# Kernel optimization log

Measured on AMD Instinct MI355X. Metric: run time of the kernel, lower is better.

Reference implementation:

```python
import jax, jax.numpy as jnp
import numpy as np

B, S, D = 4, 2048, 1024
EPS = 1e-6


def setup_inputs() -> dict:
    key = jax.random.key(0)
    ks = jax.random.split(key, 9)
    s = 1.0 / np.sqrt(D)
    return {
        "context": jax.random.normal(ks[0], (B, S, D), jnp.float32),
        "eos_mask": jax.random.randint(ks[1], (B, S, S), 0, 2, dtype=jnp.int32),
        "prior": jax.random.uniform(ks[2], (B, S, S), jnp.float32),
        "Wq": jax.random.uniform(ks[3], (D, D), jnp.float32, -s, s),
        "bq": jax.random.uniform(ks[4], (D,), jnp.float32, -s, s),
        "Wk": jax.random.uniform(ks[5], (D, D), jnp.float32, -s, s),
        "bk": jax.random.uniform(ks[6], (D,), jnp.float32, -s, s),
        "gamma": jnp.ones((D,), jnp.float32),
        "beta": jnp.zeros((D,), jnp.float32),
    }


def reference(context, eos_mask, prior, Wq, bq, Wk, bk, gamma, beta):
    d = context.shape[-1]
    seq = context.shape[1]

    # LayerNorm with torch's unbiased std (Bessel correction)
    mean = jnp.mean(context, axis=-1, keepdims=True)
    var = jnp.sum((context - mean) ** 2, axis=-1, keepdims=True) / (d - 1)
    x = gamma * (context - mean) / (jnp.sqrt(var) + EPS) + beta

    q = x @ Wq + bq  # linear_query
    k = x @ Wk + bk  # linear_key

    scores = jnp.einsum("bid,bjd->bij", q, k) / d  # note: /d, not /sqrt(d)

    idx = jnp.arange(seq)
    band = jnp.abs(idx[:, None] - idx[None, :]) == 1      # a + c (tridiagonal off-diagonals)
    sup = (idx[None, :] - idx[:, None]) == 1              # a (superdiagonal)
    strict_upper = idx[:, None] < idx[None, :]            # triu(ones) - eye
    eye = idx[:, None] == idx[None, :]

    mask = (eos_mask != 0) & band[None]                   # eos_mask & (a + c)
    scores = jnp.where(mask, scores, -1e9)
    na = jax.nn.softmax(scores, axis=-1)
    na = jnp.sqrt(na * jnp.swapaxes(na, -1, -2) + 1e-9)
    na = prior + (1.0 - prior) * na                       # hier_add_index branch

    # t = log(na+eps).masked_fill(a==0,0) @ triu  ==  cumsum along last axis
    t = jnp.where(sup[None], jnp.log(na + 1e-9), 0.0)
    t = jnp.cumsum(t, axis=-1)
    # g = triu @ t  ==  reversed cumsum along axis -2
    g = jnp.cumsum(t[..., ::-1, :], axis=-2)[..., ::-1, :]
    g = jnp.where(strict_upper[None], jnp.exp(g), 0.0)

    g_attn = g + jnp.swapaxes(g, -1, -2) + jnp.where(eye[None], na, 1e-9)
    return (g_attn, na)
```

## Files before the change

kernel.cpp:

```cpp
#include <hip/hip_runtime.h>
#include <hip/hip_bf16.h>
#include <cmath>

#define BB 4
#define SS 2048
#define DD 1024
#define BS (BB*SS)
constexpr float EPS = 1e-6f;

typedef __attribute__((ext_vector_type(8))) short short8;
typedef __attribute__((ext_vector_type(4))) float floatx4;

__device__ inline float bf2f(unsigned short u) {
    unsigned v = ((unsigned)u) << 16;
    float f; __builtin_memcpy(&f, &v, 4);
    return f;
}

__global__ __launch_bounds__(256)
void prep_kernel(const float* __restrict__ Wq, const float* __restrict__ Wk,
                 const float* __restrict__ bq, const float* __restrict__ bk,
                 __hip_bfloat16* __restrict__ Wb, float* __restrict__ u,
                 float* __restrict__ v, float* __restrict__ cs,
                 float* __restrict__ sacc) {
    int blk = blockIdx.x;
    if (blk < 2048) {
        int idx = blk * 256 + threadIdx.x;
        const int half = DD * DD / 4;
        const float* src = (idx < half) ? Wk : Wq;
        int off = (idx < half) ? idx : idx - half;
        float4 val = ((const float4*)src)[off];
        union { ushort4 uu; __hip_bfloat16 h[4]; } pk;
        pk.h[0] = __float2bfloat16(val.x);
        pk.h[1] = __float2bfloat16(val.y);
        pk.h[2] = __float2bfloat16(val.z);
        pk.h[3] = __float2bfloat16(val.w);
        ((ushort4*)Wb)[idx] = pk.uu;
    } else if (blk < 2561) {
        int gid = (blk - 2048) * 4 + (threadIdx.x >> 6);
        int lane = threadIdx.x & 63;
        if (gid > 2048) return;
        const float* row; const float* vec; float* outp;
        if (gid < 1024)      { row = Wq + (size_t)gid * DD;          vec = bk; outp = u + gid; }
        else if (gid < 2048) { row = Wk + (size_t)(gid - 1024) * DD; vec = bq; outp = v + (gid - 1024); }
        else                 { row = bq;                             vec = bk; outp = cs; }
        float s = 0.f;
        #pragma unroll
        for (int k = 0; k < 4; ++k) {
            float4 a = ((const float4*)row)[lane * 4 + k];
            float4 b = ((const float4*)vec)[lane * 4 + k];
            s += a.x * b.x + a.y * b.y + a.z * b.z + a.w * b.w;
        }
        #pragma unroll
        for (int off = 32; off; off >>= 1) s += __shfl_down(s, off);
        if (lane == 0) *outp = s;
    } else {
        int idx = (blk - 2561) * 1024 + threadIdx.x * 4;
        *(float4*)(sacc + idx) = make_float4(0.f, 0.f, 0.f, 0.f);
    }
}

__global__ __launch_bounds__(256)
void ln_kernel(const float* __restrict__ ctx, const float* __restrict__ gamma,
               const float* __restrict__ beta, const float* __restrict__ u,
               const float* __restrict__ v, const float* __restrict__ cs,
               __hip_bfloat16* __restrict__ xo, float* __restrict__ alpha,
               float* __restrict__ betav) {
    int row = blockIdx.x;
    int t = threadIdx.x;
    const float* r = ctx + (size_t)row * DD;
    float4 val = ((const float4*)r)[t];
    float s1 = val.x + val.y + val.z + val.w;
    float s2 = val.x*val.x + val.y*val.y + val.z*val.z + val.w*val.w;
    #pragma unroll
    for (int off = 32; off; off >>= 1) {
        s1 += __shfl_down(s1, off);
        s2 += __shfl_down(s2, off);
    }
    __shared__ float ls1[4], ls2[4];
    int wid = t >> 6, lane = t & 63;
    if (lane == 0) { ls1[wid] = s1; ls2[wid] = s2; }
    __syncthreads();
    if (t == 0) {
        float a = ls1[0] + ls1[1] + ls1[2] + ls1[3];
        float b = ls2[0] + ls2[1] + ls2[2] + ls2[3];
        float mean = a / DD;
        float var = (b - a * a / DD) / (DD - 1);
        ls1[0] = mean;
        ls2[0] = 1.0f / (sqrtf(var) + EPS);
    }
    __syncthreads();
    float mean = ls1[0], rstd = ls2[0];
    float4 g = ((const float4*)gamma)[t];
    float4 be = ((const float4*)beta)[t];
    float nx0 = g.x * (val.x - mean) * rstd + be.x;
    float nx1 = g.y * (val.y - mean) * rstd + be.y;
    float nx2 = g.z * (val.z - mean) * rstd + be.z;
    float nx3 = g.w * (val.w - mean) * rstd + be.w;
    union { ushort4 uu; __hip_bfloat16 h[4]; } pk;
    pk.h[0] = __float2bfloat16(nx0);
    pk.h[1] = __float2bfloat16(nx1);
    pk.h[2] = __float2bfloat16(nx2);
    pk.h[3] = __float2bfloat16(nx3);
    ((ushort4*)(xo + (size_t)row * DD))[t] = pk.uu;
    float4 u4 = ((const float4*)u)[t];
    float4 v4 = ((const float4*)v)[t];
    float du = nx0 * u4.x + nx1 * u4.y + nx2 * u4.z + nx3 * u4.w;
    float dv = nx0 * v4.x + nx1 * v4.y + nx2 * v4.z + nx3 * v4.w;
    #pragma unroll
    for (int off = 32; off; off >>= 1) {
        du += __shfl_down(du, off);
        dv += __shfl_down(dv, off);
    }
    __syncthreads();
    if (lane == 0) { ls1[wid] = du; ls2[wid] = dv; }
    __syncthreads();
    if (t == 0) {
        alpha[row] = ls1[0] + ls1[1] + ls1[2] + ls1[3] + *cs;
        betav[row] = ls2[0] + ls2[1] + ls2[2] + ls2[3];
    }
}

__global__ __launch_bounds__(256)
void gemm64_mfma(const __hip_bfloat16* __restrict__ A,
                 const __hip_bfloat16* __restrict__ B,
                 __hip_bfloat16* __restrict__ C, int ldc) {
    __shared__ short As[64 * 64];
    __shared__ short Bs[64 * 64];
    int tid = threadIdx.x;
    int wave = tid >> 6;
    int lane = tid & 63;
    int q = lane >> 4, m16 = lane & 15;
    int srow = lane >> 3;
    int skoff = (lane & 7) * 8;

    const __hip_bfloat16* gA = A + ((size_t)blockIdx.x * 64 + wave * 16 + srow) * DD + skoff;
    const __hip_bfloat16* gB = B + ((size_t)blockIdx.y * 64 + wave * 16 + srow) * DD + skoff;
    short* lA0 = As + (wave * 16) * 64;
    short* lA1 = As + (wave * 16 + 8) * 64;
    short* lB0 = Bs + (wave * 16) * 64;
    short* lB1 = Bs + (wave * 16 + 8) * 64;

    floatx4 acc[4] = {};
    for (int k0 = 0; k0 < DD; k0 += 64) {
        __builtin_amdgcn_global_load_lds(
            (const __attribute__((address_space(1))) void*)(gA + k0),
            (__attribute__((address_space(3))) void*)(lA0), 16, 0, 0);
        __builtin_amdgcn_global_load_lds(
            (const __attribute__((address_space(1))) void*)(gA + k0 + 8 * DD),
            (__attribute__((address_space(3))) void*)(lA1), 16, 0, 0);
        __builtin_amdgcn_global_load_lds(
            (const __attribute__((address_space(1))) void*)(gB + k0),
            (__attribute__((address_space(3))) void*)(lB0), 16, 0, 0);
        __builtin_amdgcn_global_load_lds(
            (const __attribute__((address_space(1))) void*)(gB + k0 + 8 * DD),
            (__attribute__((address_space(3))) void*)(lB1), 16, 0, 0);
        __syncthreads();
        #pragma unroll
        for (int h = 0; h < 2; ++h) {
            short8 af = *(const short8*)(As + (wave * 16 + m16) * 64 + h * 32 + q * 8);
            #pragma unroll
            for (int c = 0; c < 4; ++c) {
                short8 bf_ = *(const short8*)(Bs + (c * 16 + m16) * 64 + h * 32 + q * 8);
                acc[c] = __builtin_amdgcn_mfma_f32_16x16x32_bf16(af, bf_, acc[c], 0, 0, 0);
            }
        }
        __syncthreads();
    }
    #pragma unroll
    for (int c = 0; c < 4; ++c) {
        int gcol = blockIdx.y * 64 + c * 16 + m16;
        #pragma unroll
        for (int e = 0; e < 4; ++e) {
            int grow = blockIdx.x * 64 + wave * 16 + q * 4 + e;
            C[(size_t)grow * ldc + gcol] = __float2bfloat16(acc[c][e]);
        }
    }
}

#define TM 128
#define TN 128
#define TK 32
__global__ __launch_bounds__(256)
void gemm2_fused(const __hip_bfloat16* __restrict__ A,
                 const __hip_bfloat16* __restrict__ B,
                 float* __restrict__ sacc) {
    __shared__ short smem[18432];
    short* As = smem;
    short* Bs = smem + TM * TK;
    int tid = threadIdx.x;
    int wave = tid >> 6;
    int lane = tid & 63;
    int wm = wave >> 1, wn = wave & 1;
    int q = lane >> 4, m16 = lane & 15;

    int srow = lane >> 2;
    int skoff = (lane & 3) * 8;
    const __hip_bfloat16* gA = A + ((size_t)blockIdx.x * TM + wave * 32 + srow) * DD + skoff;
    const __hip_bfloat16* gB = B + ((size_t)blockIdx.y * TN + wave * 32 + srow) * DD + skoff;
    short* lAbase = As + (wave * 32) * TK;
    short* lBbase = Bs + (wave * 32) * TK;

    floatx4 acc[4][4] = {};

    for (int k0 = 0; k0 < DD; k0 += TK) {
        __builtin_amdgcn_global_load_lds(
            (const __attribute__((address_space(1))) void*)(gA + k0),
            (__attribute__((address_space(3))) void*)(lAbase), 16, 0, 0);
        __builtin_amdgcn_global_load_lds(
            (const __attribute__((address_space(1))) void*)(gA + k0 + 16 * DD),
            (__attribute__((address_space(3))) void*)(lAbase + 16 * TK), 16, 0, 0);
        __builtin_amdgcn_global_load_lds(
            (const __attribute__((address_space(1))) void*)(gB + k0),
            (__attribute__((address_space(3))) void*)(lBbase), 16, 0, 0);
        __builtin_amdgcn_global_load_lds(
            (const __attribute__((address_space(1))) void*)(gB + k0 + 16 * DD),
            (__attribute__((address_space(3))) void*)(lBbase + 16 * TK), 16, 0, 0);
        __syncthreads();
        short8 af[4], bf_[4];
        #pragma unroll
        for (int r = 0; r < 4; ++r)
            af[r] = *(const short8*)(As + (wm * 64 + r * 16 + m16) * TK + q * 8);
        #pragma unroll
        for (int c = 0; c < 4; ++c)
            bf_[c] = *(const short8*)(Bs + (wn * 64 + c * 16 + m16) * TK + q * 8);
        #pragma unroll
        for (int r = 0; r < 4; ++r)
            #pragma unroll
            for (int c = 0; c < 4; ++c)
                acc[r][c] = __builtin_amdgcn_mfma_f32_16x16x32_bf16(af[r], bf_[c], acc[r][c], 0, 0, 0);
        __syncthreads();
    }

    short* EP = smem + wave * 4608;
    #pragma unroll
    for (int r = 0; r < 4; ++r)
        #pragma unroll
        for (int c = 0; c < 4; ++c)
            #pragma unroll
            for (int e = 0; e < 4; ++e) {
                __hip_bfloat16 hv = __float2bfloat16(acc[r][c][e]);
                EP[(r * 16 + q * 4 + e) * 72 + c * 16 + m16] = *(short*)&hv;
            }

    int rl = lane;
    int growZ = blockIdx.x * TM + wm * 64 + rl;
    int gcol0 = blockIdx.y * TN + wn * 64;
    float zf[64];
    #pragma unroll
    for (int c8 = 0; c8 < 8; ++c8) {
        short8 zz = *(const short8*)(EP + rl * 72 + c8 * 8);
        #pragma unroll
        for (int e = 0; e < 8; ++e) zf[c8 * 8 + e] = bf2f((unsigned short)zz[e]);
    }
    if (growZ + 1 < BS) {
        const short8* px = (const short8*)(A + (size_t)(growZ + 1) * DD + gcol0);
        float sup = 0.f;
        #pragma unroll
        for (int c8 = 0; c8 < 8; ++c8) {
            short8 xx = px[c8];
            #pragma unroll
            for (int e = 0; e < 8; ++e) sup += zf[c8 * 8 + e] * bf2f((unsigned short)xx[e]);
        }
        atomicAdd(&sacc[growZ], sup);
    }
    if (growZ >= 1) {
        const short8* px = (const short8*)(A + (size_t)(growZ - 1) * DD + gcol0);
        float sub = 0.f;
        #pragma unroll
        for (int c8 = 0; c8 < 8; ++c8) {
            short8 xx = px[c8];
            #pragma unroll
            for (int e = 0; e < 8; ++e) sub += zf[c8 * 8 + e] * bf2f((unsigned short)xx[e]);
        }
        atomicAdd(&sacc[BS + growZ], sub);
    }
}

__global__ __launch_bounds__(256)
void softmax_kernel(const float* __restrict__ sacc, const int* __restrict__ eos,
                    const float* __restrict__ alpha, const float* __restrict__ betav,
                    float* __restrict__ vsub, float* __restrict__ vsup,
                    float* __restrict__ wuni) {
    int gw = blockIdx.x * 256 + threadIdx.x;
    int i = gw & (SS - 1);
    float a = alpha[gw];
    float ssup = 0.f, ssub = 0.f;
    if (i < SS - 1) ssup = (sacc[gw] + a + betav[gw + 1]) * (1.0f / DD);
    if (i > 0)      ssub = (sacc[BS + gw] + a + betav[gw - 1]) * (1.0f / DD);
    bool msub = (i > 0) && (eos[(size_t)gw * SS + (i - 1)] != 0);
    bool msup = (i < SS - 1) && (eos[(size_t)gw * SS + (i + 1)] != 0);
    float vs, vp, w;
    if (msub && msup) {
        float mx = fmaxf(ssub, ssup);
        float e1 = expf(ssub - mx), e2 = expf(ssup - mx);
        float inv = 1.0f / (e1 + e2);
        vs = e1 * inv; vp = e2 * inv; w = 0.f;
    } else if (msub) { vs = 1.f; vp = 0.f; w = 0.f; }
    else if (msup)   { vs = 0.f; vp = 1.f; w = 0.f; }
    else             { vs = vp = w = 1.0f / SS; }
    vsub[gw] = vs; vsup[gw] = vp; wuni[gw] = w;
}

__global__ __launch_bounds__(256)
void scan_kernel(const float* __restrict__ prior, const float* __restrict__ vsub,
                 const float* __restrict__ vsup, double* __restrict__ Lc) {
    int b = blockIdx.x;
    int t = threadIdx.x;
    double loc[8];
    double s = 0.0;
    #pragma unroll
    for (int k = 0; k < 8; ++k) {
        int tt = t * 8 + k;
        double Lv = 0.0;
        if (tt < SS - 1) {
            float pr = prior[((size_t)(b * SS + tt)) * SS + tt + 1];
            float na2 = sqrtf(vsup[b * SS + tt] * vsub[b * SS + tt + 1] + 1e-9f);
            float P = pr + (1.f - pr) * na2;
            Lv = log((double)P + 1e-9);
        }
        loc[k] = Lv; s += Lv;
    }
    __shared__ double sa[256], sb[256];
    sa[t] = s;
    __syncthreads();
    double* src = sa; double* dst = sb;
    for (int off = 1; off < 256; off <<= 1) {
        double v = src[t];
        if (t >= off) v += src[t - off];
        __syncthreads();
        dst[t] = v;
        __syncthreads();
        double* tmp = src; src = dst; dst = tmp;
    }
    double run = (t == 0) ? 0.0 : src[t - 1];
    #pragma unroll
    for (int k = 0; k < 8; ++k) {
        int idx = t * 8 + k;
        Lc[b * SS + idx] = run;
        run += loc[k];
    }
}

__global__ __launch_bounds__(256)
void out_kernel(const float* __restrict__ prior, const float* __restrict__ vsub,
                const float* __restrict__ vsup, const float* __restrict__ wuni,
                const double* __restrict__ Lc, float* __restrict__ out_g,
                float* __restrict__ out_na) {
    size_t gid = (size_t)blockIdx.x * 256 + threadIdx.x;
    int jt = (int)(gid & 511);
    int row = (int)(gid >> 9);
    int i = row & (SS - 1);
    int b = row >> 11;
    int j0 = jt * 4;
    size_t base = (size_t)row * SS + j0;
    float4 pr4 = *(const float4*)(prior + base);
    float4 wj4 = *(const float4*)(wuni + b * SS + j0);
    float pra[4] = {pr4.x, pr4.y, pr4.z, pr4.w};
    float wja[4] = {wj4.x, wj4.y, wj4.z, wj4.w};
    float wi = wuni[row];
    double Lci = Lc[row];
    const double* Lcb = Lc + b * SS;
    float nav[4], gv[4];
    #pragma unroll
    for (int c = 0; c < 4; ++c) {
        int j = j0 + c;
        float prod;
        if (j == i - 1)      prod = vsub[row] * vsup[row - 1];
        else if (j == i + 1) prod = vsup[row] * vsub[row + 1];
        else if (j == i)     prod = wi * wi;
        else                 prod = wi * wja[c];
        float na2 = sqrtf(prod + 1e-9f);
        float p = pra[c];
        float na3 = p + (1.f - p) * na2;
        nav[c] = na3;
        if (j == i) {
            gv[c] = na3;
        } else {
            double d = (j > i) ? (Lcb[j] - Lci) : (Lci - Lcb[j]);
            gv[c] = expf((float)d) + 1e-9f;
        }
    }
    *(float4*)(out_g + base) = make_float4(gv[0], gv[1], gv[2], gv[3]);
    *(float4*)(out_na + base) = make_float4(nav[0], nav[1], nav[2], nav[3]);
}

extern "C" void kernel_launch(void* const* d_in, const int* in_sizes, int n_in,
                              void* d_out, int out_size, void* d_ws, size_t ws_size,
                              hipStream_t stream) {
    const float* ctx   = (const float*)d_in[0];
    const int*   eos   = (const int*)d_in[1];
    const float* prior = (const float*)d_in[2];
    const float* Wq    = (const float*)d_in[3];
    const float* bq    = (const float*)d_in[4];
    const float* Wk    = (const float*)d_in[5];
    const float* bk    = (const float*)d_in[6];
    const float* gamma = (const float*)d_in[7];
    const float* beta  = (const float*)d_in[8];

    float* out_g  = (float*)d_out;
    float* out_na = out_g + (size_t)BB * SS * SS;

    char* ws = (char*)d_ws;
    size_t o = 0;
    __hip_bfloat16* x  = (__hip_bfloat16*)(ws + o); o += (size_t)BS * DD * 2;
    __hip_bfloat16* Wb = (__hip_bfloat16*)(ws + o); o += (size_t)2 * DD * DD * 2;
    __hip_bfloat16* Mt = (__hip_bfloat16*)(ws + o); o += (size_t)DD * DD * 2;
    double* Lc   = (double*)(ws + o); o += (size_t)BS * 8;
    float* u     = (float*)(ws + o);  o += DD * 4;
    float* v     = (float*)(ws + o);  o += DD * 4;
    float* cs    = (float*)(ws + o);  o += 64;
    float* alpha = (float*)(ws + o);  o += (size_t)BS * 4;
    float* betav = (float*)(ws + o);  o += (size_t)BS * 4;
    float* vsub  = (float*)(ws + o);  o += (size_t)BS * 4;
    float* vsup  = (float*)(ws + o);  o += (size_t)BS * 4;
    float* wuni  = (float*)(ws + o);  o += (size_t)BS * 4;
    float* sacc  = (float*)(ws + o);  o += (size_t)2 * BS * 4;

    __hip_bfloat16* Wk_bf = Wb;
    __hip_bfloat16* Wq_bf = Wb + (size_t)DD * DD;

    prep_kernel<<<2577, 256, 0, stream>>>(Wq, Wk, bq, bk, Wb, u, v, cs, sacc);
    ln_kernel<<<BS, 256, 0, stream>>>(ctx, gamma, beta, u, v, cs, x, alpha, betav);

    dim3 g1(DD / 64, DD / 64);
    gemm64_mfma<<<g1, 256, 0, stream>>>(Wk_bf, Wq_bf, Mt, DD);

    dim3 g2(BS / TM, DD / TN);
    gemm2_fused<<<g2, 256, 0, stream>>>(x, Mt, sacc);

    softmax_kernel<<<BS / 256, 256, 0, stream>>>(sacc, eos, alpha, betav, vsub, vsup, wuni);

    scan_kernel<<<BB, 256, 0, stream>>>(prior, vsub, vsup, Lc);

    size_t total = (size_t)BB * SS * SS / 4;
    out_kernel<<<(int)(total / 256), 256, 0, stream>>>(prior, vsub, vsup, wuni, Lc,
                                                       out_g, out_na);
}
```

Baseline: 327.1 us.

## Double-buffer LDS with larger K tile in fused GEMM and stream epilogue

```diff
diff --git a/kernel.cpp b/kernel.cpp
--- a/kernel.cpp
+++ b/kernel.cpp
@@ -180,57 +180,71 @@
 
 #define TM 128
 #define TN 128
-#define TK 32
+#define BK 64
 __global__ __launch_bounds__(256)
 void gemm2_fused(const __hip_bfloat16* __restrict__ A,
                  const __hip_bfloat16* __restrict__ B,
                  float* __restrict__ sacc) {
-    __shared__ short smem[18432];
-    short* As = smem;
-    short* Bs = smem + TM * TK;
+    __shared__ short smem[32768];
     int tid = threadIdx.x;
     int wave = tid >> 6;
     int lane = tid & 63;
     int wm = wave >> 1, wn = wave & 1;
     int q = lane >> 4, m16 = lane & 15;
 
-    int srow = lane >> 2;
-    int skoff = (lane & 3) * 8;
+    int srow = lane >> 3;
+    int skoff = (lane & 7) * 8;
     const __hip_bfloat16* gA = A + ((size_t)blockIdx.x * TM + wave * 32 + srow) * DD + skoff;
     const __hip_bfloat16* gB = B + ((size_t)blockIdx.y * TN + wave * 32 + srow) * DD + skoff;
-    short* lAbase = As + (wave * 32) * TK;
-    short* lBbase = Bs + (wave * 32) * TK;
 
     floatx4 acc[4][4] = {};
 
-    for (int k0 = 0; k0 < DD; k0 += TK) {
-        __builtin_amdgcn_global_load_lds(
-            (const __attribute__((address_space(1))) void*)(gA + k0),
-            (__attribute__((address_space(3))) void*)(lAbase), 16, 0, 0);
-        __builtin_amdgcn_global_load_lds(
-            (const __attribute__((address_space(1))) void*)(gA + k0 + 16 * DD),
-            (__attribute__((address_space(3))) void*)(lAbase + 16 * TK), 16, 0, 0);
-        __builtin_amdgcn_global_load_lds(
-            (const __attribute__((address_space(1))) void*)(gB + k0),
-            (__attribute__((address_space(3))) void*)(lBbase), 16, 0, 0);
-        __builtin_amdgcn_global_load_lds(
-            (const __attribute__((address_space(1))) void*)(gB + k0 + 16 * DD),
-            (__attribute__((address_space(3))) void*)(lBbase + 16 * TK), 16, 0, 0);
-        __syncthreads();
-        short8 af[4], bf_[4];
-        #pragma unroll
-        for (int r = 0; r < 4; ++r)
-            af[r] = *(const short8*)(As + (wm * 64 + r * 16 + m16) * TK + q * 8);
-        #pragma unroll
-        for (int c = 0; c < 4; ++c)
-            bf_[c] = *(const short8*)(Bs + (wn * 64 + c * 16 + m16) * TK + q * 8);
-        #pragma unroll
-        for (int r = 0; r < 4; ++r)
-            #pragma unroll
-            for (int c = 0; c < 4; ++c)
-                acc[r][c] = __builtin_amdgcn_mfma_f32_16x16x32_bf16(af[r], bf_[c], acc[r][c], 0, 0, 0);
-        __syncthreads();
-    }
+    #define STAGE(p, k0) do {                                                        \
+        short* As_ = smem + (p) * 16384;                                             \
+        short* Bs_ = As_ + 8192;                                                     \
+        _Pragma("unroll")                                                            \
+        for (int i_ = 0; i_ < 4; ++i_) {                                             \
+            __builtin_amdgcn_global_load_lds(                                        \
+                (const __attribute__((address_space(1))) void*)(gA + (k0) + i_ * 8 * DD), \
+                (__attribute__((address_space(3))) void*)(As_ + (wave * 32 + i_ * 8) * BK), 16, 0, 0); \
+            __builtin_amdgcn_global_load_lds(                                        \
+                (const __attribute__((address_space(1))) void*)(gB + (k0) + i_ * 8 * DD), \
+                (__attribute__((address_space(3))) void*)(Bs_ + (wave * 32 + i_ * 8) * BK), 16, 0, 0); \
+        }                                                                            \
+    } while (0)
+
+    #define COMPUTE(p) do {                                                          \
+        const short* As_ = smem + (p) * 16384;                                       \
+        const short* Bs_ = As_ + 8192;                                               \
+        _Pragma("unroll")                                                            \
+        for (int kk = 0; kk < 2; ++kk) {                                             \
+            short8 af[4], bfr[4];                                                    \
+            _Pragma("unroll")                                                        \
+            for (int r = 0; r < 4; ++r)                                              \
+                af[r] = *(const short8*)(As_ + (wm * 64 + r * 16 + m16) * BK + kk * 32 + q * 8); \
+            _Pragma("unroll")                                                        \
+            for (int c = 0; c < 4; ++c)                                              \
+                bfr[c] = *(const short8*)(Bs_ + (wn * 64 + c * 16 + m16) * BK + kk * 32 + q * 8); \
+            _Pragma("unroll")                                                        \
+            for (int r = 0; r < 4; ++r)                                              \
+                _Pragma("unroll")                                                    \
+                for (int c = 0; c < 4; ++c)                                          \
+                    acc[r][c] = __builtin_amdgcn_mfma_f32_16x16x32_bf16(af[r], bfr[c], acc[r][c], 0, 0, 0); \
+        }                                                                            \
+    } while (0)
+
+    STAGE(0, 0);
+    __syncthreads();
+    for (int t = 0; t < DD / BK; t += 2) {
+        if (t + 1 < DD / BK) STAGE(1, (t + 1) * BK);
+        COMPUTE(0);
+        __syncthreads();
+        if (t + 2 < DD / BK) STAGE(0, (t + 2) * BK);
+        COMPUTE(1);
+        __syncthreads();
+    }
+    #undef STAGE
+    #undef COMPUTE
 
     short* EP = smem + wave * 4608;
     #pragma unroll
@@ -246,35 +260,30 @@
     int rl = lane;
     int growZ = blockIdx.x * TM + wm * 64 + rl;
     int gcol0 = blockIdx.y * TN + wn * 64;
-    float zf[64];
+    bool hs = (growZ + 1 < BS);
+    bool hb = (growZ >= 1);
+    const short8* psup = (const short8*)(A + (size_t)(growZ + 1) * DD + gcol0);
+    const short8* psub = (const short8*)(A + (size_t)(growZ - 1) * DD + gcol0);
+    float sup = 0.f, sub = 0.f;
     #pragma unroll
     for (int c8 = 0; c8 < 8; ++c8) {
         short8 zz = *(const short8*)(EP + rl * 72 + c8 * 8);
-        #pragma unroll
-        for (int e = 0; e < 8; ++e) zf[c8 * 8 + e] = bf2f((unsigned short)zz[e]);
-    }
-    if (growZ + 1 < BS) {
-        const short8* px = (const short8*)(A + (size_t)(growZ + 1) * DD + gcol0);
-        float sup = 0.f;
-        #pragma unroll
-        for (int c8 = 0; c8 < 8; ++c8) {
-            short8 xx = px[c8];
+        float zf[8];
+        #pragma unroll
+        for (int e = 0; e < 8; ++e) zf[e] = bf2f((unsigned short)zz[e]);
+        if (hs) {
+            short8 xx = psup[c8];
             #pragma unroll
-            for (int e = 0; e < 8; ++e) sup += zf[c8 * 8 + e] * bf2f((unsigned short)xx[e]);
-        }
-        atomicAdd(&sacc[growZ], sup);
-    }
-    if (growZ >= 1) {
-        const short8* px = (const short8*)(A + (size_t)(growZ - 1) * DD + gcol0);
-        float sub = 0.f;
-        #pragma unroll
-        for (int c8 = 0; c8 < 8; ++c8) {
-            short8 xx = px[c8];
+            for (int e = 0; e < 8; ++e) sup += zf[e] * bf2f((unsigned short)xx[e]);
+        }
+        if (hb) {
+            short8 xx = psub[c8];
             #pragma unroll
-            for (int e = 0; e < 8; ++e) sub += zf[c8 * 8 + e] * bf2f((unsigned short)xx[e]);
-        }
-        atomicAdd(&sacc[BS + growZ], sub);
-    }
+            for (int e = 0; e < 8; ++e) sub += zf[e] * bf2f((unsigned short)xx[e]);
+        }
+    }
+    if (hs) atomicAdd(&sacc[growZ], sup);
+    if (hb) atomicAdd(&sacc[BS + growZ], sub);
 }
 
 __global__ __launch_bounds__(256)
```

Result: no change. 328.8 us (+0.5%).
